# Kernel optimization log

Measured on AMD Instinct MI355X. Metric: run time of the kernel, lower is better.

The kernel has to match this reference:

```python
import jax, jax.numpy as jnp
import numpy as np

N_NODES = 100000
N_EDGES = 1600000
IN_DIM = 256
HID = 64
OUT_DIM = 1
N_GRAPHS = 100


def setup_inputs() -> dict:
    key = jax.random.key(0)
    ks = jax.random.split(key, 12)
    x = jax.random.normal(ks[0], (N_NODES, IN_DIM), dtype=jnp.float32)
    edge_index = jax.random.randint(ks[1], (2, N_EDGES), 0, N_NODES, dtype=jnp.int64 if jax.config.read('jax_enable_x64') else jnp.int32)
    batch = jnp.sort(jax.random.randint(ks[2], (N_NODES,), 0, N_GRAPHS, dtype=jnp.int32))
    def lin(k, fan_in, fan_out):
        bound = 1.0 / np.sqrt(fan_in)
        kw, kb = jax.random.split(k)
        W = jax.random.uniform(kw, (fan_in, fan_out), minval=-bound, maxval=bound, dtype=jnp.float32)
        b = jax.random.uniform(kb, (fan_out,), minval=-bound, maxval=bound, dtype=jnp.float32)
        return W, b
    W1, b1 = lin(ks[3], IN_DIM, HID)
    W2, b2 = lin(ks[4], HID, HID)
    W3, b3 = lin(ks[5], HID, HID)
    Wl, bl = lin(ks[6], HID, OUT_DIM)
    return {"x": x, "edge_index": edge_index, "batch": batch,
            "W1": W1, "b1": b1, "W2": W2, "b2": b2, "W3": W3, "b3": b3,
            "Wl": Wl, "bl": bl}


def _gcn_layer(h, src, dst, norm, W, b):
    # PyG GCNConv: h' = scatter_add(norm * (h @ W)[src] -> dst) + b
    h = h @ W                                   # [N, F_out]
    msg = h[src] * norm[:, None]                # [E+N, F_out] irregular gather
    agg = jax.ops.segment_sum(msg, dst, num_segments=N_NODES)
    return agg + b


def reference(x, edge_index, batch, W1, b1, W2, b2, W3, b3, Wl, bl):
    # add self loops (static shape) as GCNConv does by default
    loops = jnp.arange(N_NODES, dtype=edge_index.dtype)
    src = jnp.concatenate([edge_index[0], loops])  # [E+N]
    dst = jnp.concatenate([edge_index[1], loops])  # [E+N]
    # symmetric normalization: deg over targets incl. self loops
    deg = jax.ops.segment_sum(jnp.ones_like(dst, dtype=x.dtype), dst, num_segments=N_NODES)
    dinv = jnp.where(deg > 0, jax.lax.rsqrt(deg), 0.0)
    norm = dinv[src] * dinv[dst]                # [E+N]

    h = jax.nn.relu(_gcn_layer(x, src, dst, norm, W1, b1))
    h = jax.nn.relu(_gcn_layer(h, src, dst, norm, W2, b2))
    h = _gcn_layer(h, src, dst, norm, W3, b3)   # last conv: no relu

    # global_add_pool over graphs; dropout is identity at inference
    pooled = jax.ops.segment_sum(h, batch, num_segments=N_GRAPHS)  # [G, HID]
    return pooled @ Wl + bl                     # [G, 1]
```

## Files before the change

kernel.cpp:

```cpp
#include <hip/hip_runtime.h>

#define N_NODES 100000
#define N_EDGES 1600000
#define IN_DIM 256
#define HID 64
#define N_GRAPHS 100
#define BSHIFT 8
#define NBUCK 391
#define CHUNK 4096
#define BCAP 5120

typedef __attribute__((ext_vector_type(8))) short short8;
typedef __attribute__((ext_vector_type(8))) unsigned short us8;
typedef __attribute__((ext_vector_type(4))) float floatx4;
typedef __attribute__((ext_vector_type(2))) float floatx2;

__device__ __forceinline__ unsigned short f2b(float f) {
    unsigned int u = __float_as_uint(f);
    unsigned int r = (u + 0x7FFFu + ((u >> 16) & 1u)) >> 16;
    return (unsigned short)r;
}
__device__ __forceinline__ float b2f(unsigned short b) {
    return __uint_as_float(((unsigned int)b) << 16);
}
__device__ __forceinline__ unsigned char f2e4m3(float f) {
    return (unsigned char)(__builtin_amdgcn_cvt_pk_fp8_f32(f, 0.f, 0, false) & 0xFF);
}


__global__ void k_prep(const float* __restrict__ W1, const float* __restrict__ W2,
                       const float* __restrict__ W3, const float* __restrict__ Wl,
                       const float* __restrict__ b3,
                       unsigned short* __restrict__ wt1, unsigned short* __restrict__ wt2,
                       float* __restrict__ w3l,
                       int* __restrict__ bcnt, float* __restrict__ partial) {
    int i = blockIdx.x * 256 + threadIdx.x;
    if (i < IN_DIM * HID) {
        int k = i >> 6, n = i & 63;
        wt1[n * IN_DIM + k] = f2b(W1[i]);
    }
    if (i < HID * HID) {
        int k = i >> 6, n = i & 63;
        wt2[n * HID + k] = f2b(W2[i]);
    }
    if (i < NBUCK) bcnt[i] = 0;
    if (i < N_GRAPHS * 256) partial[i] = 0.f;
    if (blockIdx.x == 0) {
        int t = threadIdx.x;
        if (t < HID) {
            float s = 0.f;
            for (int n = 0; n < HID; ++n) s += W3[t * HID + n] * Wl[n];
            w3l[t] = s;
        } else if (t == HID) {
            float s = 0.f;
            for (int n = 0; n < HID; ++n) s += b3[n] * Wl[n];
            w3l[HID] = s;
        }
    }
}


__global__ __launch_bounds__(256) void k_scatter(const int* __restrict__ src,
                                                 const int* __restrict__ dst,
                                                 int* __restrict__ bcnt,
                                                 int* __restrict__ ebuckF) {
    __shared__ int lc[NBUCK];
    const int b = blockIdx.x, t = threadIdx.x;
    for (int i = t; i < NBUCK; i += 256) lc[i] = 0;
    __syncthreads();
    const int base = b * CHUNK;
    int pk[16], bk[16], rk[16];
#pragma unroll
    for (int i = 0; i < 16; ++i) {
        int e = base + i * 256 + t;
        rk[i] = -1;
        if (e < N_EDGES) {
            int s = src[e], d = dst[e];
            bk[i] = d >> BSHIFT;
            pk[i] = (s << BSHIFT) | (d & 255);
            rk[i] = atomicAdd(&lc[bk[i]], 1);
        }
    }
    __syncthreads();
    for (int i = t; i < NBUCK; i += 256)
        lc[i] = lc[i] ? atomicAdd(&bcnt[i], lc[i]) : 0;
    __syncthreads();
#pragma unroll
    for (int i = 0; i < 16; ++i)
        if (rk[i] >= 0) {
            int p = lc[bk[i]] + rk[i];
            if (p < BCAP) ebuckF[bk[i] * BCAP + p] = pk[i];
        }
}


__global__ __launch_bounds__(256) void k_dgemm1(const int* __restrict__ bcnt,
                                                const int* __restrict__ ebuckF,
                                                int* __restrict__ deg,
                                                float* __restrict__ dinv,
                                                int* __restrict__ rowptr,
                                                int* __restrict__ colF,
                                                const float* __restrict__ X,
                                                const unsigned short* __restrict__ Wt,
                                                unsigned char* __restrict__ Tb8) {
    __shared__ unsigned short Wb[64][264];
    const int t = threadIdx.x;

    if (blockIdx.x < NBUCK) {
        int* ld = (int*)&Wb[0][0];
        int* sA = ld + 256;
        int* lf = sA + 256;
        const int b = blockIdx.x;
        const int cnt = min(bcnt[b], BCAP);
        const int ebase = b * BCAP;
        ld[t] = 1;
        __syncthreads();
        for (int j = t; j < cnt; j += 256) atomicAdd(&ld[ebuckF[ebase + j] & 255], 1);
        __syncthreads();
        const int node = (b << BSHIFT) + t;
        const int dg = ld[t];
        if (node < N_NODES) {
            deg[node] = dg;
            dinv[node] = rsqrtf((float)dg);
        }
        const int c = (node < N_NODES) ? dg - 1 : 0;
        sA[t] = c;
        __syncthreads();
        for (int off = 1; off < 256; off <<= 1) {
            int u = (t >= off) ? sA[t - off] : 0;
            __syncthreads();
            sA[t] += u;
            __syncthreads();
        }
        const int pos = ebase + sA[t] - c;
        if (node < N_NODES) rowptr[node] = pos;
        lf[t] = pos;
        __syncthreads();
        for (int j = t; j < cnt; j += 256) {
            int v = ebuckF[ebase + j];
            int p = atomicAdd(&lf[v & 255], 1);
            colF[p] = v >> BSHIFT;
        }
        return;
    }

    const int lane = t & 63, wv = t >> 6;
    const int fl = lane & 15, quad = lane >> 4;
    const int r0 = (blockIdx.x - NBUCK) * 64;

    for (int g = t; g < 64 * 32; g += 256) {
        int n = g >> 5, kc8 = g & 31;
        *(us8*)&Wb[n][kc8 * 8] = *(const us8*)(Wt + n * IN_DIM + kc8 * 8);
    }

    const int arow = r0 + wv * 16 + fl;
    const bool valid = arow < N_NODES;
    const float* xp = X + (size_t)(valid ? arow : 0) * IN_DIM;

    floatx4 acc[4];
#pragma unroll
    for (int j = 0; j < 4; ++j) acc[j] = (floatx4){0.f, 0.f, 0.f, 0.f};

    __syncthreads();

#pragma unroll
    for (int kc = 0; kc < IN_DIM; kc += 32) {
        float4 x0 = make_float4(0.f, 0.f, 0.f, 0.f);
        float4 x1 = make_float4(0.f, 0.f, 0.f, 0.f);
        if (valid) {
            x0 = *(const float4*)(xp + kc + quad * 8);
            x1 = *(const float4*)(xp + kc + quad * 8 + 4);
        }
        short8 a;
        a[0] = (short)f2b(x0.x); a[1] = (short)f2b(x0.y);
        a[2] = (short)f2b(x0.z); a[3] = (short)f2b(x0.w);
        a[4] = (short)f2b(x1.x); a[5] = (short)f2b(x1.y);
        a[6] = (short)f2b(x1.z); a[7] = (short)f2b(x1.w);
#pragma unroll
        for (int ct = 0; ct < 4; ++ct) {
            short8 b = *(const short8*)&Wb[ct * 16 + fl][kc + quad * 8];
            acc[ct] = __builtin_amdgcn_mfma_f32_16x16x32_bf16(a, b, acc[ct], 0, 0, 0);
        }
    }

    int rbase = r0 + wv * 16 + quad * 4;
#pragma unroll
    for (int r = 0; r < 4; ++r) {
        int row = rbase + r;
        if (row < N_NODES) {
#pragma unroll
            for (int ct = 0; ct < 4; ++ct)
                Tb8[(size_t)row * HID + ct * 16 + fl] = f2e4m3(acc[ct][r]);
        }
    }
}


__global__ __launch_bounds__(1024) void k_aggmm2(const unsigned char* __restrict__ Tb8,
                                                 const int* __restrict__ rowptr,
                                                 const int* __restrict__ deg,
                                                 const float* __restrict__ dinv,
                                                 const int* __restrict__ col,
                                                 const float* __restrict__ bias,
                                                 const unsigned short* __restrict__ Wt,
                                                 unsigned short* __restrict__ Tb2) {
    __shared__ unsigned short Wb[64][72];
    __shared__ unsigned short Hs[16][72];
    const int t = threadIdx.x;
    const int lane = t & 63, wv = t >> 6;
    const int grp = lane >> 3, fl8 = lane & 7;

    for (int g = t; g < 64 * 8; g += 1024) {
        int n = g >> 3, kc8 = g & 7;
        *(us8*)&Wb[n][kc8 * 8] = *(const us8*)(Wt + n * HID + kc8 * 8);
    }

    const int node = blockIdx.x * 16 + wv;
    int e = __builtin_amdgcn_readfirstlane(rowptr[node]);
    const int end = e + __builtin_amdgcn_readfirstlane(deg[node]) - 1;
    const float di = dinv[node];
    float a0 = 0.f, a1 = 0.f, a2 = 0.f, a3 = 0.f;
    float a4 = 0.f, a5 = 0.f, a6 = 0.f, a7 = 0.f;

#define ACC_FP8(dv, vx, vy)                                                 \
    {                                                                       \
        floatx2 p0 = __builtin_amdgcn_cvt_pk_f32_fp8((int)(vx), false);     \
        floatx2 p1 = __builtin_amdgcn_cvt_pk_f32_fp8((int)(vx), true);      \
        floatx2 p2 = __builtin_amdgcn_cvt_pk_f32_fp8((int)(vy), false);     \
        floatx2 p3 = __builtin_amdgcn_cvt_pk_f32_fp8((int)(vy), true);      \
        a0 = fmaf(dv, p0.x, a0); a1 = fmaf(dv, p0.y, a1);                   \
        a2 = fmaf(dv, p1.x, a2); a3 = fmaf(dv, p1.y, a3);                   \
        a4 = fmaf(dv, p2.x, a4); a5 = fmaf(dv, p2.y, a5);                   \
        a6 = fmaf(dv, p3.x, a6); a7 = fmaf(dv, p3.y, a7);                   \
    }

    for (; e + 16 <= end; e += 16) {
        int s0 = col[e + grp];
        int s1 = col[e + 8 + grp];
        float dv0 = dinv[s0], dv1 = dinv[s1];
        uint2 t0 = *(const uint2*)(Tb8 + (size_t)s0 * HID + fl8 * 8);
        uint2 t1 = *(const uint2*)(Tb8 + (size_t)s1 * HID + fl8 * 8);
        ACC_FP8(dv0, t0.x, t0.y);
        ACC_FP8(dv1, t1.x, t1.y);
    }
    for (; e + 8 <= end; e += 8) {
        int s = col[e + grp];
        float dv = dinv[s];
        uint2 tv = *(const uint2*)(Tb8 + (size_t)s * HID + fl8 * 8);
        ACC_FP8(dv, tv.x, tv.y);
    }
    if (e + grp < end) {
        int s = col[e + grp];
        float dv = dinv[s];
        uint2 tv = *(const uint2*)(Tb8 + (size_t)s * HID + fl8 * 8);
        ACC_FP8(dv, tv.x, tv.y);
    }
    a0 += __shfl_xor(a0, 8);  a1 += __shfl_xor(a1, 8);
    a2 += __shfl_xor(a2, 8);  a3 += __shfl_xor(a3, 8);
    a4 += __shfl_xor(a4, 8);  a5 += __shfl_xor(a5, 8);
    a6 += __shfl_xor(a6, 8);  a7 += __shfl_xor(a7, 8);
    a0 += __shfl_xor(a0, 16); a1 += __shfl_xor(a1, 16);
    a2 += __shfl_xor(a2, 16); a3 += __shfl_xor(a3, 16);
    a4 += __shfl_xor(a4, 16); a5 += __shfl_xor(a5, 16);
    a6 += __shfl_xor(a6, 16); a7 += __shfl_xor(a7, 16);
    a0 += __shfl_xor(a0, 32); a1 += __shfl_xor(a1, 32);
    a2 += __shfl_xor(a2, 32); a3 += __shfl_xor(a3, 32);
    a4 += __shfl_xor(a4, 32); a5 += __shfl_xor(a5, 32);
    a6 += __shfl_xor(a6, 32); a7 += __shfl_xor(a7, 32);
    {
        uint2 sv = *(const uint2*)(Tb8 + (size_t)node * HID + fl8 * 8);
        ACC_FP8(di, sv.x, sv.y);
    }
#undef ACC_FP8
    float4 b0 = *(const float4*)(bias + fl8 * 8);
    float4 b1v = *(const float4*)(bias + fl8 * 8 + 4);
    a0 = fmaxf(fmaf(di, a0, b0.x), 0.f);
    a1 = fmaxf(fmaf(di, a1, b0.y), 0.f);
    a2 = fmaxf(fmaf(di, a2, b0.z), 0.f);
    a3 = fmaxf(fmaf(di, a3, b0.w), 0.f);
    a4 = fmaxf(fmaf(di, a4, b1v.x), 0.f);
    a5 = fmaxf(fmaf(di, a5, b1v.y), 0.f);
    a6 = fmaxf(fmaf(di, a6, b1v.z), 0.f);
    a7 = fmaxf(fmaf(di, a7, b1v.w), 0.f);
    if (grp == 0) {
        us8 o;
        o[0] = f2b(a0); o[1] = f2b(a1); o[2] = f2b(a2); o[3] = f2b(a3);
        o[4] = f2b(a4); o[5] = f2b(a5); o[6] = f2b(a6); o[7] = f2b(a7);
        *(us8*)&Hs[wv][fl8 * 8] = o;
    }
    __syncthreads();

    if (wv == 0) {
        const int fl = lane & 15, quad = lane >> 4;
        floatx4 acc[4];
#pragma unroll
        for (int j = 0; j < 4; ++j) acc[j] = (floatx4){0.f, 0.f, 0.f, 0.f};
#pragma unroll
        for (int kc = 0; kc < HID; kc += 32) {
            short8 a = *(const short8*)&Hs[fl][kc + quad * 8];
#pragma unroll
            for (int ct = 0; ct < 4; ++ct) {
                short8 b = *(const short8*)&Wb[ct * 16 + fl][kc + quad * 8];
                acc[ct] = __builtin_amdgcn_mfma_f32_16x16x32_bf16(a, b, acc[ct], 0, 0, 0);
            }
        }
        int rbase = blockIdx.x * 16 + quad * 4;
#pragma unroll
        for (int r = 0; r < 4; ++r) {
            int row = rbase + r;
            float di2 = dinv[row];
#pragma unroll
            for (int ct = 0; ct < 4; ++ct)
                Tb2[(size_t)row * HID + ct * 16 + fl] = f2b(di2 * acc[ct][r]);
        }
    }
}


__global__ __launch_bounds__(1024) void k_agg_z(const unsigned short* __restrict__ Tb,
                                                const int* __restrict__ rowptr,
                                                const int* __restrict__ deg,
                                                const float* __restrict__ dinv,
                                                const int* __restrict__ col,
                                                const float* __restrict__ bias,
                                                const float* __restrict__ w3l,
                                                float* __restrict__ z) {
    int lane = threadIdx.x & 63;
    int node = blockIdx.x * 16 + (threadIdx.x >> 6);
    int grp = lane >> 3, fl = lane & 7;
    int e = __builtin_amdgcn_readfirstlane(rowptr[node]);
    int end = e + __builtin_amdgcn_readfirstlane(deg[node]) - 1;
    float a0 = 0.f, a1 = 0.f, a2 = 0.f, a3 = 0.f;
    float a4 = 0.f, a5 = 0.f, a6 = 0.f, a7 = 0.f;
    for (; e + 16 <= end; e += 16) {
        int s0 = col[e + grp];
        int s1 = col[e + 8 + grp];
        us8 t0 = *(const us8*)(Tb + (size_t)s0 * HID + fl * 8);
        us8 t1 = *(const us8*)(Tb + (size_t)s1 * HID + fl * 8);
        a0 += b2f(t0[0]) + b2f(t1[0]); a1 += b2f(t0[1]) + b2f(t1[1]);
        a2 += b2f(t0[2]) + b2f(t1[2]); a3 += b2f(t0[3]) + b2f(t1[3]);
        a4 += b2f(t0[4]) + b2f(t1[4]); a5 += b2f(t0[5]) + b2f(t1[5]);
        a6 += b2f(t0[6]) + b2f(t1[6]); a7 += b2f(t0[7]) + b2f(t1[7]);
    }
    for (; e + 8 <= end; e += 8) {
        int s = col[e + grp];
        us8 tv = *(const us8*)(Tb + (size_t)s * HID + fl * 8);
        a0 += b2f(tv[0]); a1 += b2f(tv[1]); a2 += b2f(tv[2]); a3 += b2f(tv[3]);
        a4 += b2f(tv[4]); a5 += b2f(tv[5]); a6 += b2f(tv[6]); a7 += b2f(tv[7]);
    }
    if (e + grp < end) {
        int s = col[e + grp];
        us8 tv = *(const us8*)(Tb + (size_t)s * HID + fl * 8);
        a0 += b2f(tv[0]); a1 += b2f(tv[1]); a2 += b2f(tv[2]); a3 += b2f(tv[3]);
        a4 += b2f(tv[4]); a5 += b2f(tv[5]); a6 += b2f(tv[6]); a7 += b2f(tv[7]);
    }
    a0 += __shfl_xor(a0, 8);  a1 += __shfl_xor(a1, 8);
    a2 += __shfl_xor(a2, 8);  a3 += __shfl_xor(a3, 8);
    a4 += __shfl_xor(a4, 8);  a5 += __shfl_xor(a5, 8);
    a6 += __shfl_xor(a6, 8);  a7 += __shfl_xor(a7, 8);
    a0 += __shfl_xor(a0, 16); a1 += __shfl_xor(a1, 16);
    a2 += __shfl_xor(a2, 16); a3 += __shfl_xor(a3, 16);
    a4 += __shfl_xor(a4, 16); a5 += __shfl_xor(a5, 16);
    a6 += __shfl_xor(a6, 16); a7 += __shfl_xor(a7, 16);
    a0 += __shfl_xor(a0, 32); a1 += __shfl_xor(a1, 32);
    a2 += __shfl_xor(a2, 32); a3 += __shfl_xor(a3, 32);
    a4 += __shfl_xor(a4, 32); a5 += __shfl_xor(a5, 32);
    a6 += __shfl_xor(a6, 32); a7 += __shfl_xor(a7, 32);
    us8 sv = *(const us8*)(Tb + (size_t)node * HID + fl * 8);
    a0 += b2f(sv[0]); a1 += b2f(sv[1]); a2 += b2f(sv[2]); a3 += b2f(sv[3]);
    a4 += b2f(sv[4]); a5 += b2f(sv[5]); a6 += b2f(sv[6]); a7 += b2f(sv[7]);
    float di = dinv[node];
    float4 b0 = *(const float4*)(bias + fl * 8);
    float4 b1v = *(const float4*)(bias + fl * 8 + 4);
    a0 = fmaxf(fmaf(di, a0, b0.x), 0.f);
    a1 = fmaxf(fmaf(di, a1, b0.y), 0.f);
    a2 = fmaxf(fmaf(di, a2, b0.z), 0.f);
    a3 = fmaxf(fmaf(di, a3, b0.w), 0.f);
    a4 = fmaxf(fmaf(di, a4, b1v.x), 0.f);
    a5 = fmaxf(fmaf(di, a5, b1v.y), 0.f);
    a6 = fmaxf(fmaf(di, a6, b1v.z), 0.f);
    a7 = fmaxf(fmaf(di, a7, b1v.w), 0.f);
    float4 w0 = *(const float4*)(w3l + fl * 8);
    float4 w1v = *(const float4*)(w3l + fl * 8 + 4);
    float s = a0 * w0.x + a1 * w0.y + a2 * w0.z + a3 * w0.w +
              a4 * w1v.x + a5 * w1v.y + a6 * w1v.z + a7 * w1v.w;
    s += __shfl_xor(s, 1);
    s += __shfl_xor(s, 2);
    s += __shfl_xor(s, 4);
    if (lane == 0) z[node] = di * s;
}

__global__ __launch_bounds__(256) void k_aggpool_s(const float* __restrict__ z,
                                                   const int* __restrict__ rowptr,
                                                   const int* __restrict__ deg,
                                                   const float* __restrict__ dinv,
                                                   const int* __restrict__ col,
                                                   const float* __restrict__ w3l,
                                                   const int* __restrict__ batch,
                                                   float* __restrict__ partial) {
    int i = blockIdx.x * 256 + threadIdx.x;
    if (i >= N_NODES) return;
    int e = rowptr[i];
    int end = e + deg[i] - 1;
    float s0 = z[i], s1 = 0.f, s2 = 0.f, s3 = 0.f;
    for (; e + 4 <= end; e += 4) {
        s0 += z[col[e]];
        s1 += z[col[e + 1]];
        s2 += z[col[e + 2]];
        s3 += z[col[e + 3]];
    }
    for (; e < end; ++e) s0 += z[col[e]];
    float s = w3l[HID] + dinv[i] * (s0 + s1 + s2 + s3);
    atomicAdd(&partial[batch[i] * 256 + (blockIdx.x & 255)], s);
}

__global__ void k_pool_reduce(const float* __restrict__ partial,
                              const float* __restrict__ bl,
                              float* __restrict__ out) {
    int g = blockIdx.x, t = threadIdx.x;
    float s = partial[g * 256 + t];
    s += __shfl_xor(s, 32);
    s += __shfl_xor(s, 16);
    s += __shfl_xor(s, 8);
    s += __shfl_xor(s, 4);
    s += __shfl_xor(s, 2);
    s += __shfl_xor(s, 1);
    __shared__ float ws[4];
    if ((t & 63) == 0) ws[t >> 6] = s;
    __syncthreads();
    if (t == 0) out[g] = bl[0] + ws[0] + ws[1] + ws[2] + ws[3];
}

extern "C" void kernel_launch(void* const* d_in, const int* in_sizes, int n_in,
                              void* d_out, int out_size, void* d_ws, size_t ws_size,
                              hipStream_t stream) {
    const float* x     = (const float*)d_in[0];
    const int*   ei    = (const int*)d_in[1];
    const int*   batch = (const int*)d_in[2];
    const float* W1    = (const float*)d_in[3];
    const float* b1    = (const float*)d_in[4];
    const float* W2    = (const float*)d_in[5];
    const float* b2    = (const float*)d_in[6];
    const float* W3    = (const float*)d_in[7];
    const float* b3    = (const float*)d_in[8];
    const float* Wl    = (const float*)d_in[9];
    const float* bl    = (const float*)d_in[10];
    float* out = (float*)d_out;

    char* p = (char*)d_ws;
    unsigned char*  tb8 = (unsigned char*)p;  p += (size_t)N_NODES * HID;
    unsigned short* hB  = (unsigned short*)p; p += (size_t)N_NODES * HID * 2;
    int*   colF    = (int*)p;   p += (size_t)NBUCK * BCAP * 4;
    int*   ebuckF  = (int*)p;   p += (size_t)NBUCK * BCAP * 4;
    int*   deg     = (int*)p;   p += (size_t)N_NODES * 4;
    float* dinv    = (float*)p; p += (size_t)N_NODES * 4;
    int*   rowptr  = (int*)p;   p += (size_t)N_NODES * 4;
    float* z       = (float*)p; p += (size_t)N_NODES * 4;
    int*   bcnt    = (int*)p;   p += (NBUCK + 1) * 4;
    float* partial = (float*)p; p += (size_t)N_GRAPHS * 256 * 4;
    unsigned short* wt1 = (unsigned short*)p; p += (size_t)IN_DIM * HID * 2;
    unsigned short* wt2 = (unsigned short*)p; p += (size_t)HID * HID * 2;
    float* w3l     = (float*)p; p += 128 * 4;

    const int* src  = ei;
    const int* dstp = ei + N_EDGES;

    const int nb = (N_NODES + 255) / 256;
    const int cb = (N_EDGES + CHUNK - 1) / CHUNK;
    const int gemm_blocks = (N_NODES + 63) / 64;
    const int agg_blocks = N_NODES / 16;

    k_prep<<<128, 256, 0, stream>>>(W1, W2, W3, Wl, b3, wt1, wt2, w3l, bcnt, partial);
    k_scatter<<<cb, 256, 0, stream>>>(src, dstp, bcnt, ebuckF);
    k_dgemm1<<<NBUCK + gemm_blocks, 256, 0, stream>>>(bcnt, ebuckF, deg, dinv, rowptr,
                                                      colF, x, wt1, tb8);

    k_aggmm2<<<agg_blocks, 1024, 0, stream>>>(tb8, rowptr, deg, dinv, colF, b1, wt2, hB);
    k_agg_z<<<agg_blocks, 1024, 0, stream>>>(hB, rowptr, deg, dinv, colF, b2, w3l, z);

    k_aggpool_s<<<nb, 256, 0, stream>>>(z, rowptr, deg, dinv, colF, w3l, batch, partial);
    k_pool_reduce<<<N_GRAPHS, 256, 0, stream>>>(partial, bl, out);
}
```

Before: 352.1 us.

## Pre-scale layer-1 output by dinv, store layer-2 features in fp8, count degrees globally

```diff
diff --git a/kernel.cpp b/kernel.cpp
--- a/kernel.cpp
+++ b/kernel.cpp
@@ -28,12 +28,17 @@
 }
 
 
-__global__ void k_prep(const float* __restrict__ W1, const float* __restrict__ W2,
-                       const float* __restrict__ W3, const float* __restrict__ Wl,
-                       const float* __restrict__ b3,
-                       unsigned short* __restrict__ wt1, unsigned short* __restrict__ wt2,
-                       float* __restrict__ w3l,
-                       int* __restrict__ bcnt, float* __restrict__ partial) {
+__global__ __launch_bounds__(256) void k_prep(const float* __restrict__ W1,
+                                              const float* __restrict__ W2,
+                                              const float* __restrict__ W3,
+                                              const float* __restrict__ Wl,
+                                              const float* __restrict__ b3,
+                                              unsigned short* __restrict__ wt1,
+                                              unsigned short* __restrict__ wt2,
+                                              float* __restrict__ w3l,
+                                              int* __restrict__ bcnt,
+                                              int* __restrict__ deg,
+                                              float* __restrict__ partial) {
     int i = blockIdx.x * 256 + threadIdx.x;
     if (i < IN_DIM * HID) {
         int k = i >> 6, n = i & 63;
@@ -44,6 +49,7 @@
         wt2[n * HID + k] = f2b(W2[i]);
     }
     if (i < NBUCK) bcnt[i] = 0;
+    if (i < N_NODES) deg[i] = 0;
     if (i < N_GRAPHS * 256) partial[i] = 0.f;
     if (blockIdx.x == 0) {
         int t = threadIdx.x;
@@ -63,7 +69,8 @@
 __global__ __launch_bounds__(256) void k_scatter(const int* __restrict__ src,
                                                  const int* __restrict__ dst,
                                                  int* __restrict__ bcnt,
-                                                 int* __restrict__ ebuckF) {
+                                                 int* __restrict__ ebuckF,
+                                                 int* __restrict__ deg) {
     __shared__ int lc[NBUCK];
     const int b = blockIdx.x, t = threadIdx.x;
     for (int i = t; i < NBUCK; i += 256) lc[i] = 0;
@@ -79,6 +86,7 @@
             bk[i] = d >> BSHIFT;
             pk[i] = (s << BSHIFT) | (d & 255);
             rk[i] = atomicAdd(&lc[bk[i]], 1);
+            atomicAdd(&deg[d], 1);
         }
     }
     __syncthreads();
@@ -96,7 +104,7 @@
 
 __global__ __launch_bounds__(256) void k_dgemm1(const int* __restrict__ bcnt,
                                                 const int* __restrict__ ebuckF,
-                                                int* __restrict__ deg,
+                                                const int* __restrict__ deg,
                                                 float* __restrict__ dinv,
                                                 int* __restrict__ rowptr,
                                                 int* __restrict__ colF,
@@ -113,17 +121,12 @@
         const int b = blockIdx.x;
         const int cnt = min(bcnt[b], BCAP);
         const int ebase = b * BCAP;
-        ld[t] = 1;
+        ld[t] = 0;
         __syncthreads();
         for (int j = t; j < cnt; j += 256) atomicAdd(&ld[ebuckF[ebase + j] & 255], 1);
         __syncthreads();
         const int node = (b << BSHIFT) + t;
-        const int dg = ld[t];
-        if (node < N_NODES) {
-            deg[node] = dg;
-            dinv[node] = rsqrtf((float)dg);
-        }
-        const int c = (node < N_NODES) ? dg - 1 : 0;
+        const int c = (node < N_NODES) ? ld[t] : 0;
         sA[t] = c;
         __syncthreads();
         for (int off = 1; off < 256; off <<= 1) {
@@ -188,12 +191,24 @@
     for (int r = 0; r < 4; ++r) {
         int row = rbase + r;
         if (row < N_NODES) {
+            float di = rsqrtf((float)(deg[row] + 1));
+            dinv[row] = di;
 #pragma unroll
             for (int ct = 0; ct < 4; ++ct)
-                Tb8[(size_t)row * HID + ct * 16 + fl] = f2e4m3(acc[ct][r]);
-        }
-    }
-}
+                Tb8[(size_t)row * HID + ct * 16 + fl] = f2e4m3(di * acc[ct][r]);
+        }
+    }
+}
+
+#define ACC8(vx, vy)                                                    \
+    {                                                                   \
+        floatx2 p0 = __builtin_amdgcn_cvt_pk_f32_fp8((int)(vx), false); \
+        floatx2 p1 = __builtin_amdgcn_cvt_pk_f32_fp8((int)(vx), true);  \
+        floatx2 p2 = __builtin_amdgcn_cvt_pk_f32_fp8((int)(vy), false); \
+        floatx2 p3 = __builtin_amdgcn_cvt_pk_f32_fp8((int)(vy), true);  \
+        a0 += p0.x; a1 += p0.y; a2 += p1.x; a3 += p1.y;                 \
+        a4 += p2.x; a5 += p2.y; a6 += p3.x; a7 += p3.y;                 \
+    }
 
 
 __global__ __launch_bounds__(1024) void k_aggmm2(const unsigned char* __restrict__ Tb8,
@@ -203,7 +218,7 @@
                                                  const int* __restrict__ col,
                                                  const float* __restrict__ bias,
                                                  const unsigned short* __restrict__ Wt,
-                                                 unsigned short* __restrict__ Tb2) {
+                                                 unsigned char* __restrict__ Tb2_8) {
     __shared__ unsigned short Wb[64][72];
     __shared__ unsigned short Hs[16][72];
     const int t = threadIdx.x;
@@ -217,43 +232,28 @@
 
     const int node = blockIdx.x * 16 + wv;
     int e = __builtin_amdgcn_readfirstlane(rowptr[node]);
-    const int end = e + __builtin_amdgcn_readfirstlane(deg[node]) - 1;
+    const int end = e + __builtin_amdgcn_readfirstlane(deg[node]);
     const float di = dinv[node];
     float a0 = 0.f, a1 = 0.f, a2 = 0.f, a3 = 0.f;
     float a4 = 0.f, a5 = 0.f, a6 = 0.f, a7 = 0.f;
 
-#define ACC_FP8(dv, vx, vy)                                                 \
-    {                                                                       \
-        floatx2 p0 = __builtin_amdgcn_cvt_pk_f32_fp8((int)(vx), false);     \
-        floatx2 p1 = __builtin_amdgcn_cvt_pk_f32_fp8((int)(vx), true);      \
-        floatx2 p2 = __builtin_amdgcn_cvt_pk_f32_fp8((int)(vy), false);     \
-        floatx2 p3 = __builtin_amdgcn_cvt_pk_f32_fp8((int)(vy), true);      \
-        a0 = fmaf(dv, p0.x, a0); a1 = fmaf(dv, p0.y, a1);                   \
-        a2 = fmaf(dv, p1.x, a2); a3 = fmaf(dv, p1.y, a3);                   \
-        a4 = fmaf(dv, p2.x, a4); a5 = fmaf(dv, p2.y, a5);                   \
-        a6 = fmaf(dv, p3.x, a6); a7 = fmaf(dv, p3.y, a7);                   \
-    }
-
     for (; e + 16 <= end; e += 16) {
         int s0 = col[e + grp];
         int s1 = col[e + 8 + grp];
-        float dv0 = dinv[s0], dv1 = dinv[s1];
         uint2 t0 = *(const uint2*)(Tb8 + (size_t)s0 * HID + fl8 * 8);
         uint2 t1 = *(const uint2*)(Tb8 + (size_t)s1 * HID + fl8 * 8);
-        ACC_FP8(dv0, t0.x, t0.y);
-        ACC_FP8(dv1, t1.x, t1.y);
+        ACC8(t0.x, t0.y);
+        ACC8(t1.x, t1.y);
     }
     for (; e + 8 <= end; e += 8) {
         int s = col[e + grp];
-        float dv = dinv[s];
         uint2 tv = *(const uint2*)(Tb8 + (size_t)s * HID + fl8 * 8);
-        ACC_FP8(dv, tv.x, tv.y);
+        ACC8(tv.x, tv.y);
     }
     if (e + grp < end) {
         int s = col[e + grp];
-        float dv = dinv[s];
         uint2 tv = *(const uint2*)(Tb8 + (size_t)s * HID + fl8 * 8);
-        ACC_FP8(dv, tv.x, tv.y);
+        ACC8(tv.x, tv.y);
     }
     a0 += __shfl_xor(a0, 8);  a1 += __shfl_xor(a1, 8);
     a2 += __shfl_xor(a2, 8);  a3 += __shfl_xor(a3, 8);
@@ -269,9 +269,8 @@
     a6 += __shfl_xor(a6, 32); a7 += __shfl_xor(a7, 32);
     {
         uint2 sv = *(const uint2*)(Tb8 + (size_t)node * HID + fl8 * 8);
-        ACC_FP8(di, sv.x, sv.y);
-    }
-#undef ACC_FP8
+        ACC8(sv.x, sv.y);
+    }
     float4 b0 = *(const float4*)(bias + fl8 * 8);
     float4 b1v = *(const float4*)(bias + fl8 * 8 + 4);
     a0 = fmaxf(fmaf(di, a0, b0.x), 0.f);
@@ -311,13 +310,13 @@
             float di2 = dinv[row];
 #pragma unroll
             for (int ct = 0; ct < 4; ++ct)
-                Tb2[(size_t)row * HID + ct * 16 + fl] = f2b(di2 * acc[ct][r]);
-        }
-    }
-}
-
-
-__global__ __launch_bounds__(1024) void k_agg_z(const unsigned short* __restrict__ Tb,
+                Tb2_8[(size_t)row * HID + ct * 16 + fl] = f2e4m3(di2 * acc[ct][r]);
+        }
+    }
+}
+
+
+__global__ __launch_bounds__(1024) void k_agg_z(const unsigned char* __restrict__ Tb8,
                                                 const int* __restrict__ rowptr,
                                                 const int* __restrict__ deg,
                                                 const float* __restrict__ dinv,
@@ -329,30 +328,26 @@
     int node = blockIdx.x * 16 + (threadIdx.x >> 6);
     int grp = lane >> 3, fl = lane & 7;
     int e = __builtin_amdgcn_readfirstlane(rowptr[node]);
-    int end = e + __builtin_amdgcn_readfirstlane(deg[node]) - 1;
+    int end = e + __builtin_amdgcn_readfirstlane(deg[node]);
     float a0 = 0.f, a1 = 0.f, a2 = 0.f, a3 = 0.f;
     float a4 = 0.f, a5 = 0.f, a6 = 0.f, a7 = 0.f;
     for (; e + 16 <= end; e += 16) {
         int s0 = col[e + grp];
         int s1 = col[e + 8 + grp];
-        us8 t0 = *(const us8*)(Tb + (size_t)s0 * HID + fl * 8);
-        us8 t1 = *(const us8*)(Tb + (size_t)s1 * HID + fl * 8);
-        a0 += b2f(t0[0]) + b2f(t1[0]); a1 += b2f(t0[1]) + b2f(t1[1]);
-        a2 += b2f(t0[2]) + b2f(t1[2]); a3 += b2f(t0[3]) + b2f(t1[3]);
-        a4 += b2f(t0[4]) + b2f(t1[4]); a5 += b2f(t0[5]) + b2f(t1[5]);
-        a6 += b2f(t0[6]) + b2f(t1[6]); a7 += b2f(t0[7]) + b2f(t1[7]);
+        uint2 t0 = *(const uint2*)(Tb8 + (size_t)s0 * HID + fl * 8);
+        uint2 t1 = *(const uint2*)(Tb8 + (size_t)s1 * HID + fl * 8);
+        ACC8(t0.x, t0.y);
+        ACC8(t1.x, t1.y);
     }
     for (; e + 8 <= end; e += 8) {
         int s = col[e + grp];
-        us8 tv = *(const us8*)(Tb + (size_t)s * HID + fl * 8);
-        a0 += b2f(tv[0]); a1 += b2f(tv[1]); a2 += b2f(tv[2]); a3 += b2f(tv[3]);
-        a4 += b2f(tv[4]); a5 += b2f(tv[5]); a6 += b2f(tv[6]); a7 += b2f(tv[7]);
+        uint2 tv = *(const uint2*)(Tb8 + (size_t)s * HID + fl * 8);
+        ACC8(tv.x, tv.y);
     }
     if (e + grp < end) {
         int s = col[e + grp];
-        us8 tv = *(const us8*)(Tb + (size_t)s * HID + fl * 8);
-        a0 += b2f(tv[0]); a1 += b2f(tv[1]); a2 += b2f(tv[2]); a3 += b2f(tv[3]);
-        a4 += b2f(tv[4]); a5 += b2f(tv[5]); a6 += b2f(tv[6]); a7 += b2f(tv[7]);
+        uint2 tv = *(const uint2*)(Tb8 + (size_t)s * HID + fl * 8);
+        ACC8(tv.x, tv.y);
     }
     a0 += __shfl_xor(a0, 8);  a1 += __shfl_xor(a1, 8);
     a2 += __shfl_xor(a2, 8);  a3 += __shfl_xor(a3, 8);
@@ -366,9 +361,10 @@
     a2 += __shfl_xor(a2, 32); a3 += __shfl_xor(a3, 32);
     a4 += __shfl_xor(a4, 32); a5 += __shfl_xor(a5, 32);
     a6 += __shfl_xor(a6, 32); a7 += __shfl_xor(a7, 32);
-    us8 sv = *(const us8*)(Tb + (size_t)node * HID + fl * 8);
-    a0 += b2f(sv[0]); a1 += b2f(sv[1]); a2 += b2f(sv[2]); a3 += b2f(sv[3]);
-    a4 += b2f(sv[4]); a5 += b2f(sv[5]); a6 += b2f(sv[6]); a7 += b2f(sv[7]);
+    {
+        uint2 sv = *(const uint2*)(Tb8 + (size_t)node * HID + fl * 8);
+        ACC8(sv.x, sv.y);
+    }
     float di = dinv[node];
     float4 b0 = *(const float4*)(bias + fl * 8);
     float4 b1v = *(const float4*)(bias + fl * 8 + 4);
@@ -389,6 +385,7 @@
     s += __shfl_xor(s, 4);
     if (lane == 0) z[node] = di * s;
 }
+#undef ACC8
 
 __global__ __launch_bounds__(256) void k_aggpool_s(const float* __restrict__ z,
                                                    const int* __restrict__ rowptr,
@@ -401,7 +398,7 @@
     int i = blockIdx.x * 256 + threadIdx.x;
     if (i >= N_NODES) return;
     int e = rowptr[i];
-    int end = e + deg[i] - 1;
+    int end = e + deg[i];
     float s0 = z[i], s1 = 0.f, s2 = 0.f, s3 = 0.f;
     for (; e + 4 <= end; e += 4) {
         s0 += z[col[e]];
@@ -449,7 +446,7 @@
 
     char* p = (char*)d_ws;
     unsigned char*  tb8 = (unsigned char*)p;  p += (size_t)N_NODES * HID;
-    unsigned short* hB  = (unsigned short*)p; p += (size_t)N_NODES * HID * 2;
+    unsigned char*  hB8 = (unsigned char*)p;  p += (size_t)N_NODES * HID;
     int*   colF    = (int*)p;   p += (size_t)NBUCK * BCAP * 4;
     int*   ebuckF  = (int*)p;   p += (size_t)NBUCK * BCAP * 4;
     int*   deg     = (int*)p;   p += (size_t)N_NODES * 4;
@@ -470,13 +467,13 @@
     const int gemm_blocks = (N_NODES + 63) / 64;
     const int agg_blocks = N_NODES / 16;
 
-    k_prep<<<128, 256, 0, stream>>>(W1, W2, W3, Wl, b3, wt1, wt2, w3l, bcnt, partial);
-    k_scatter<<<cb, 256, 0, stream>>>(src, dstp, bcnt, ebuckF);
+    k_prep<<<nb, 256, 0, stream>>>(W1, W2, W3, Wl, b3, wt1, wt2, w3l, bcnt, deg, partial);
+    k_scatter<<<cb, 256, 0, stream>>>(src, dstp, bcnt, ebuckF, deg);
     k_dgemm1<<<NBUCK + gemm_blocks, 256, 0, stream>>>(bcnt, ebuckF, deg, dinv, rowptr,
                                                       colF, x, wt1, tb8);
 
-    k_aggmm2<<<agg_blocks, 1024, 0, stream>>>(tb8, rowptr, deg, dinv, colF, b1, wt2, hB);
-    k_agg_z<<<agg_blocks, 1024, 0, stream>>>(hB, rowptr, deg, dinv, colF, b2, w3l, z);
+    k_aggmm2<<<agg_blocks, 1024, 0, stream>>>(tb8, rowptr, deg, dinv, colF, b1, wt2, hB8);
+    k_agg_z<<<agg_blocks, 1024, 0, stream>>>(hB8, rowptr, deg, dinv, colF, b2, w3l, z);
 
     k_aggpool_s<<<nb, 256, 0, stream>>>(z, rowptr, deg, dinv, colF, w3l, batch, partial);
     k_pool_reduce<<<N_GRAPHS, 256, 0, stream>>>(partial, bl, out);
```

New measurement: 399.1 us. 13.4% more time.
